# Kernel tuning notes

Hardware: AMD Instinct MI355X
Metric: run time of the kernel (lower is better)

The kernel has to match this reference:

```python
import jax, jax.numpy as jnp
import numpy as np

B, T, TS, J, D, H = 4, 512, 512, 17, 256, 8
CD = D // H
SCALE = CD ** -0.5


def setup_inputs() -> dict:
    key = jax.random.key(0)
    ks = jax.random.split(key, 7)
    return {
        "q": jax.random.normal(ks[0], (B, T, J, D), dtype=jnp.float32),
        "kv": jax.random.normal(ks[1], (B, TS, J, D), dtype=jnp.float32),
        "Wq": jax.random.normal(ks[2], (D, D), dtype=jnp.float32) * (D ** -0.5),
        "Wk": jax.random.normal(ks[3], (D, D), dtype=jnp.float32) * (D ** -0.5),
        "Wv": jax.random.normal(ks[4], (D, D), dtype=jnp.float32) * (D ** -0.5),
        "Wp": jax.random.normal(ks[5], (D, D), dtype=jnp.float32) * (D ** -0.5),
        "bp": jnp.zeros((D,), dtype=jnp.float32),
    }


def reference(q, kv, Wq, Wk, Wv, Wp, bp):
    b, t, j, d = q.shape
    t_sup = kv.shape[1]
    h, cd = H, CD
    # linear projections (torch Linear: x @ W^T), split heads -> [b,h,j,t,cd]
    qh = (q @ Wq.T).reshape(b, t, j, h, cd).transpose(0, 3, 2, 1, 4)
    kh = (kv @ Wk.T).reshape(b, t_sup, j, h, cd).transpose(0, 3, 2, 1, 4)
    vh = (kv @ Wv.T).reshape(b, t_sup, j, h, cd).transpose(0, 3, 2, 1, 4)
    # full attention matrix over temporal axes: [b,h,j,t,t_sup]
    scores = jnp.einsum("bhjtc,bhjsc->bhjts", qh, kh) * SCALE
    attn = jax.nn.softmax(scores, axis=-1)
    out = jnp.einsum("bhjts,bhjsc->bhjtc", attn, vh)
    out = out.transpose(0, 3, 2, 1, 4).reshape(b, t, j, d)  # [b,t,j,d]
    return out @ Wp.T + bp
```

## Files before the change

kernel.cpp:

```cpp
#include <hip/hip_runtime.h>
#include <hip/hip_bf16.h>

#define BB 4
#define TT 512
#define JJ 17
#define DD 256
#define HH 8
#define MROWS (BB*TT*JJ)
#define SZE ((size_t)MROWS * DD)
#define WSZ (DD*DD)
#define QSCALE 0.2550265247510319f
#define RST (17*256)

typedef short v8s __attribute__((ext_vector_type(8)));
typedef float v4f __attribute__((ext_vector_type(4)));

__device__ __forceinline__ unsigned short f2bf(float f) {
    union { float f; unsigned int u; } c; c.f = f;
    unsigned int u = c.u;
    return (unsigned short)((u + 0x7FFF + ((u >> 16) & 1)) >> 16);
}
__device__ __forceinline__ unsigned int pkbf(float lo, float hi) {
    union { float f; unsigned int u; } a, b; a.f = lo; b.f = hi;
    return __builtin_amdgcn_perm(b.u + 0x8000u, a.u + 0x8000u, 0x07060302u);
}
__device__ __forceinline__ float fexp2(float x) {
    return __builtin_amdgcn_exp2f(x);
}

__device__ __forceinline__ void gld16(const unsigned short* g, unsigned short* l) {
    __builtin_amdgcn_global_load_lds(
        (const __attribute__((address_space(1))) void*)g,
        (__attribute__((address_space(3))) void*)l,
        16, 0, 0);
}

__global__ __launch_bounds__(256) void prep_kernel(
    const float* __restrict__ q, const float* __restrict__ kv,
    const float* __restrict__ Wq, const float* __restrict__ Wk,
    const float* __restrict__ Wv, const float* __restrict__ Wp,
    unsigned short* __restrict__ qb, unsigned short* __restrict__ kvb,
    unsigned short* __restrict__ Wqb, unsigned short* __restrict__ Wkb,
    unsigned short* __restrict__ Wvb, unsigned short* __restrict__ Wpb)
{
    size_t i = ((size_t)blockIdx.x * 256 + threadIdx.x) * 8;
    const float* src; unsigned short* dst; size_t off; float scale = 1.f;
    if (i < SZE)            { src = q;  dst = qb;  off = i;        scale = QSCALE; }
    else if (i < 2 * SZE)   { src = kv; dst = kvb; off = i - SZE; }
    else {
        size_t k = i - 2 * SZE;
        int w = (int)(k >> 16);
        off = k & (WSZ - 1);
        src = (w == 0) ? Wq : (w == 1) ? Wk : (w == 2) ? Wv : Wp;
        dst = (w == 0) ? Wqb : (w == 1) ? Wkb : (w == 2) ? Wvb : Wpb;
    }
    float4 x0 = *(const float4*)(src + off);
    float4 x1 = *(const float4*)(src + off + 4);
    union { unsigned short s[8]; int4 v; } u;
    u.s[0] = f2bf(x0.x * scale); u.s[1] = f2bf(x0.y * scale);
    u.s[2] = f2bf(x0.z * scale); u.s[3] = f2bf(x0.w * scale);
    u.s[4] = f2bf(x1.x * scale); u.s[5] = f2bf(x1.y * scale);
    u.s[6] = f2bf(x1.z * scale); u.s[7] = f2bf(x1.w * scale);
    *(int4*)(dst + off) = u.v;
}

__global__ __launch_bounds__(512) void gemm_kernel(
    const unsigned short* __restrict__ A0,
    const unsigned short* __restrict__ A1,
    const unsigned short* __restrict__ A2,
    const unsigned short* __restrict__ W0,
    const unsigned short* __restrict__ W1,
    const unsigned short* __restrict__ W2,
    unsigned short* __restrict__ Y0,
    unsigned short* __restrict__ Y1,
    unsigned short* __restrict__ Y2)
{
    const int z = blockIdx.y;
    const unsigned short* A = (z == 0) ? A0 : (z == 1) ? A1 : A2;
    const unsigned short* W = (z == 0) ? W0 : (z == 1) ? W1 : W2;
    unsigned short* Y       = (z == 0) ? Y0 : (z == 1) ? Y1 : Y2;

    const int bm = blockIdx.x;

    __shared__ unsigned short As[2][128 * 32];
    __shared__ unsigned short Bs[2][256 * 32];

    const int tid  = threadIdx.x;
    const int wv   = tid >> 6;
    const int lane = tid & 63;
    const int wm   = wv & 1;
    const int wn   = wv >> 1;
    const int quad = lane >> 4;
    const int l16  = lane & 15;

    const int s     = lane >> 2;
    const int chunk = lane & 3;
    const int fsw   = (s ^ (s >> 2)) & 3;
    const int cg    = chunk ^ fsw;
    const int srow  = wv * 16 + s;
    const unsigned short* gA  = A + (size_t)(bm * 128 + srow) * 256 + cg * 8;
    const unsigned short* gB0 = W + (size_t)srow * 256 + cg * 8;
    const unsigned short* gB1 = W + (size_t)(128 + srow) * 256 + cg * 8;
    unsigned short* lA  = &As[0][wv * 512 + lane * 8];
    unsigned short* lB0 = &Bs[0][wv * 512 + lane * 8];
    unsigned short* lB1 = &Bs[0][4096 + wv * 512 + lane * 8];

    const int rch8 = (quad ^ ((l16 ^ (l16 >> 2)) & 3)) * 8;

    v4f acc[4][4] = {};

    gld16(gA,  lA);
    gld16(gB0, lB0);
    gld16(gB1, lB1);
    __syncthreads();

    for (int kt = 0; kt < 8; ++kt) {
        const int cur = kt & 1;
        if (kt < 7) {
            const int nk = (kt + 1) * 32;
            const int nb = cur ^ 1;
            gld16(gA  + nk, lA  + nb * 4096);
            gld16(gB0 + nk, lB0 + nb * 8192);
            gld16(gB1 + nk, lB1 + nb * 8192);
        }
        v8s a[4], b[4];
        #pragma unroll
        for (int i = 0; i < 4; ++i)
            a[i] = *(const v8s*)(&As[cur][(wm * 64 + i * 16 + l16) * 32 + rch8]);
        #pragma unroll
        for (int j = 0; j < 4; ++j)
            b[j] = *(const v8s*)(&Bs[cur][(wn * 64 + j * 16 + l16) * 32 + rch8]);
        #pragma unroll
        for (int i = 0; i < 4; ++i)
            #pragma unroll
            for (int j = 0; j < 4; ++j)
                acc[i][j] = __builtin_amdgcn_mfma_f32_16x16x32_bf16(
                    a[i], b[j], acc[i][j], 0, 0, 0);
        __syncthreads();
    }

    #pragma unroll
    for (int i = 0; i < 4; ++i)
        #pragma unroll
        for (int j = 0; j < 4; ++j)
            #pragma unroll
            for (int r = 0; r < 4; ++r) {
                int gm = bm * 128 + wm * 64 + i * 16 + quad * 4 + r;
                int gn = wn * 64 + j * 16 + l16;
                Y[(size_t)gm * 256 + gn] = f2bf(acc[i][j][r]);
            }
}

__global__ __launch_bounds__(256) void gemmo_kernel(
    const unsigned short* __restrict__ A,
    const unsigned short* __restrict__ W,
    const float* __restrict__ bias,
    float* __restrict__ out)
{
    const int bm = blockIdx.x;

    __shared__ unsigned short As[2][64 * 32];
    __shared__ unsigned short Bs[2][256 * 32];

    const int tid  = threadIdx.x;
    const int lane = tid & 63;
    const int wn   = tid >> 6;
    const int quad = lane >> 4;
    const int l16  = lane & 15;

    const int arow  = tid >> 2;
    const int chunk = tid & 3;
    const int cgA   = (chunk ^ ((arow ^ (arow >> 2)) & 3)) * 8;
    const unsigned short* gA = A + (size_t)(bm * 64 + arow) * 256 + cgA;
    const unsigned short* gB = W + (size_t)arow * 256 + cgA;
    unsigned short* lA = &As[0][tid * 8];
    unsigned short* lB = &Bs[0][tid * 8];

    const int rch8 = (quad ^ ((l16 ^ (l16 >> 2)) & 3)) * 8;

    v4f acc[4][4] = {};

    gld16(gA, lA);
    #pragma unroll
    for (int p = 0; p < 4; ++p)
        gld16(gB + (size_t)p * 64 * 256, lB + p * 2048);
    __syncthreads();

    for (int kt = 0; kt < 8; ++kt) {
        const int cur = kt & 1;
        if (kt < 7) {
            const int nk = (kt + 1) * 32;
            const int nb = cur ^ 1;
            gld16(gA + nk, lA + nb * 2048);
            #pragma unroll
            for (int p = 0; p < 4; ++p)
                gld16(gB + (size_t)p * 64 * 256 + nk, lB + nb * 8192 + p * 2048);
        }
        v8s a[4], b[4];
        #pragma unroll
        for (int i = 0; i < 4; ++i)
            a[i] = *(const v8s*)(&As[cur][(i * 16 + l16) * 32 + rch8]);
        #pragma unroll
        for (int j = 0; j < 4; ++j)
            b[j] = *(const v8s*)(&Bs[cur][(wn * 64 + j * 16 + l16) * 32 + rch8]);
        #pragma unroll
        for (int i = 0; i < 4; ++i)
            #pragma unroll
            for (int j = 0; j < 4; ++j)
                acc[i][j] = __builtin_amdgcn_mfma_f32_16x16x32_bf16(
                    a[i], b[j], acc[i][j], 0, 0, 0);
        __syncthreads();
    }

    #pragma unroll
    for (int i = 0; i < 4; ++i)
        #pragma unroll
        for (int j = 0; j < 4; ++j)
            #pragma unroll
            for (int r = 0; r < 4; ++r) {
                int gm = bm * 64 + i * 16 + quad * 4 + r;
                int gn = wn * 64 + j * 16 + l16;
                out[(size_t)gm * 256 + gn] = acc[i][j][r] + bias[gn];
            }
}

#define VST 136
#define PST 72

__global__ __launch_bounds__(256) void attn_kernel(
    const unsigned short* __restrict__ Qp,
    const unsigned short* __restrict__ Kp,
    const unsigned short* __restrict__ Vp,
    unsigned short* __restrict__ Att)
{
    const int id  = blockIdx.x;
    const int bjh = (id & 7) | ((id >> 5) << 3);
    const int qt  = (id >> 3) & 3;
    const int h   = bjh & 7;
    const int bj  = bjh >> 3;
    const int j   = bj % 17;
    const int b_  = bj / 17;

    __shared__ unsigned short Ks[128 * 40];
    __shared__ unsigned short Vs[32 * VST];
    __shared__ unsigned short Ps[128 * PST];
    __shared__ float Ls[128];

    const int tid  = threadIdx.x;
    const int wave = tid >> 6;
    const int lane = tid & 63;
    const int quad = lane >> 4;
    const int l16  = lane & 15;

    const int base0 = b_ * 512 * RST + j * 256 + h * 32;

    v8s qa[2];
    #pragma unroll
    for (int fi = 0; fi < 2; ++fi)
        qa[fi] = *(const v8s*)(
            Qp + base0 + (qt * 128 + wave * 32 + fi * 16 + l16) * RST + quad * 8);

    float lacc[2] = {0.f, 0.f};
    v4f accO[2][2] = {};

    for (int kc = 0; kc < 4; ++kc) {
        __syncthreads();
        #pragma unroll
        for (int c = 0; c < 2; ++c) {
            int krow = wave * 16 + l16 + c * 64;
            *(int4*)(&Ks[krow * 40 + quad * 8]) = *(const int4*)(
                Kp + base0 + (kc * 128 + krow) * RST + quad * 8);
        }
        #pragma unroll
        for (int c = 0; c < 2; ++c) {
            int idx  = c * 256 + tid;
            int srow = idx >> 2;
            int cd0  = (idx & 3) << 3;
            int xof  = (((srow >> 3) ^ (cd0 >> 3)) << 3) + (srow & 7);
            union { int4 v; unsigned short s[8]; } u;
            u.v = *(const int4*)(
                Vp + base0 + (kc * 128 + srow) * RST + cd0);
            #pragma unroll
            for (int i = 0; i < 8; ++i)
                Vs[(cd0 + i) * VST + xof] = u.s[i];
        }
        __syncthreads();

        #pragma unroll
        for (int half = 0; half < 2; ++half) {
            v4f accST[4][2] = {};
            __builtin_amdgcn_s_setprio(1);
            #pragma unroll
            for (int si = 0; si < 4; ++si) {
                v8s kb = *(const v8s*)(&Ks[((half * 4 + si) * 16 + l16) * 40 + quad * 8]);
                #pragma unroll
                for (int fi = 0; fi < 2; ++fi)
                    accST[si][fi] = __builtin_amdgcn_mfma_f32_16x16x32_bf16(
                        kb, qa[fi], accST[si][fi], 0, 0, 0);
            }
            __builtin_amdgcn_s_setprio(0);
            #pragma unroll
            for (int fi = 0; fi < 2; ++fi) {
                int prow = (wave * 32 + fi * 16 + l16) * PST;
                #pragma unroll
                for (int si = 0; si < 4; ++si) {
                    float p0 = fexp2(accST[si][fi][0]);
                    float p1 = fexp2(accST[si][fi][1]);
                    float p2 = fexp2(accST[si][fi][2]);
                    float p3 = fexp2(accST[si][fi][3]);
                    lacc[fi] += (p0 + p1) + (p2 + p3);
                    uint2 pk;
                    pk.x = pkbf(p0, p1);
                    pk.y = pkbf(p2, p3);
                    *(uint2*)(&Ps[prow + si * 16 + quad * 4]) = pk;
                }
            }
            asm volatile("s_waitcnt lgkmcnt(0)" ::: "memory");

            __builtin_amdgcn_s_setprio(1);
            #pragma unroll
            for (int ks = 0; ks < 2; ++ks) {
                v8s pa[2];
                #pragma unroll
                for (int fi = 0; fi < 2; ++fi)
                    pa[fi] = *(const v8s*)(&Ps[(wave * 32 + fi * 16 + l16) * PST +
                                               ks * 32 + quad * 8]);
                #pragma unroll
                for (int nj = 0; nj < 2; ++nj) {
                    int cd  = nj * 16 + l16;
                    int blk = (half * 8 + ks * 4 + quad) ^ (cd >> 3);
                    v8s vb = *(const v8s*)(&Vs[cd * VST + (blk << 3)]);
                    #pragma unroll
                    for (int fi = 0; fi < 2; ++fi)
                        accO[fi][nj] = __builtin_amdgcn_mfma_f32_16x16x32_bf16(
                            pa[fi], vb, accO[fi][nj], 0, 0, 0);
                }
            }
            __builtin_amdgcn_s_setprio(0);
        }
    }

    #pragma unroll
    for (int fi = 0; fi < 2; ++fi) {
        float lv = lacc[fi];
        lv += __shfl_xor(lv, 16);
        lv += __shfl_xor(lv, 32);
        if (quad == 0) Ls[wave * 32 + fi * 16 + l16] = lv;
    }
    asm volatile("s_waitcnt lgkmcnt(0)" ::: "memory");

    #pragma unroll
    for (int fi = 0; fi < 2; ++fi) {
        float4 lv = *(float4*)(&Ls[wave * 32 + fi * 16 + quad * 4]);
        float rl[4] = {1.f / lv.x, 1.f / lv.y, 1.f / lv.z, 1.f / lv.w};
        #pragma unroll
        for (int nj = 0; nj < 2; ++nj) {
            #pragma unroll
            for (int r = 0; r < 4; ++r) {
                int trow = qt * 128 + wave * 32 + fi * 16 + quad * 4 + r;
                int cd   = nj * 16 + l16;
                float v  = accO[fi][nj][r] * rl[r];
                Att[(size_t)(base0 + trow * RST + cd)] = f2bf(v);
            }
        }
    }
}

extern "C" void kernel_launch(void* const* d_in, const int* in_sizes, int n_in,
                              void* d_out, int out_size, void* d_ws, size_t ws_size,
                              hipStream_t stream) {
    const float* q  = (const float*)d_in[0];
    const float* kv = (const float*)d_in[1];
    const float* Wq = (const float*)d_in[2];
    const float* Wk = (const float*)d_in[3];
    const float* Wv = (const float*)d_in[4];
    const float* Wp = (const float*)d_in[5];
    const float* bp = (const float*)d_in[6];

    unsigned short* ws  = (unsigned short*)d_ws;
    unsigned short* Qp  = ws;
    unsigned short* Kp  = ws + SZE;
    unsigned short* Vp  = ws + 2 * SZE;
    unsigned short* qb  = ws + 3 * SZE;
    unsigned short* kvb = ws + 4 * SZE;
    unsigned short* Wqb = ws + 5 * SZE;
    unsigned short* Wkb = Wqb + WSZ;
    unsigned short* Wvb = Wkb + WSZ;
    unsigned short* Wpb = Wvb + WSZ;
    unsigned short* Att = qb;
    float* out = (float*)d_out;

    prep_kernel<<<8832, 256, 0, stream>>>(q, kv, Wq, Wk, Wv, Wp,
                                          qb, kvb, Wqb, Wkb, Wvb, Wpb);
    gemm_kernel<<<dim3(272, 3), 512, 0, stream>>>(
        qb, kvb, kvb, Wqb, Wkb, Wvb, Qp, Kp, Vp);
    attn_kernel<<<dim3(2176), 256, 0, stream>>>(Qp, Kp, Vp, Att);
    gemmo_kernel<<<dim3(544), 256, 0, stream>>>(Att, Wpb, bp, out);
}
```

Baseline: 210.1 us.

## Fuse fp32-to-bf16 activation conversion into QKV projection GEMM loads

The separate prep pass that converted q and kv to bf16 (and applied the Q scale) is removed. The QKV GEMM now reads fp32 activations directly, converts and scales them in registers, and writes them into the swizzled LDS buffer after the MFMA step so the conversion overlaps compute. Only the weight conversion stays as a small kernel. This saves a full read and write of two large activation tensors, but the A-tile loads become synchronous register loads instead of async global-to-LDS copies, and kv is read and converted twice, once for the K and once for the V projection.

```diff
diff --git a/kernel.cpp b/kernel.cpp
--- a/kernel.cpp
+++ b/kernel.cpp
@@ -35,39 +35,30 @@
         16, 0, 0);
 }
 
-__global__ __launch_bounds__(256) void prep_kernel(
-    const float* __restrict__ q, const float* __restrict__ kv,
+__global__ __launch_bounds__(256) void prepw_kernel(
     const float* __restrict__ Wq, const float* __restrict__ Wk,
     const float* __restrict__ Wv, const float* __restrict__ Wp,
-    unsigned short* __restrict__ qb, unsigned short* __restrict__ kvb,
     unsigned short* __restrict__ Wqb, unsigned short* __restrict__ Wkb,
     unsigned short* __restrict__ Wvb, unsigned short* __restrict__ Wpb)
 {
-    size_t i = ((size_t)blockIdx.x * 256 + threadIdx.x) * 8;
-    const float* src; unsigned short* dst; size_t off; float scale = 1.f;
-    if (i < SZE)            { src = q;  dst = qb;  off = i;        scale = QSCALE; }
-    else if (i < 2 * SZE)   { src = kv; dst = kvb; off = i - SZE; }
-    else {
-        size_t k = i - 2 * SZE;
-        int w = (int)(k >> 16);
-        off = k & (WSZ - 1);
-        src = (w == 0) ? Wq : (w == 1) ? Wk : (w == 2) ? Wv : Wp;
-        dst = (w == 0) ? Wqb : (w == 1) ? Wkb : (w == 2) ? Wvb : Wpb;
-    }
+    size_t k = ((size_t)blockIdx.x * 256 + threadIdx.x) * 8;
+    int w = (int)(k >> 16);
+    size_t off = k & (WSZ - 1);
+    const float* src = (w == 0) ? Wq : (w == 1) ? Wk : (w == 2) ? Wv : Wp;
+    unsigned short* dst = (w == 0) ? Wqb : (w == 1) ? Wkb : (w == 2) ? Wvb : Wpb;
     float4 x0 = *(const float4*)(src + off);
     float4 x1 = *(const float4*)(src + off + 4);
     union { unsigned short s[8]; int4 v; } u;
-    u.s[0] = f2bf(x0.x * scale); u.s[1] = f2bf(x0.y * scale);
-    u.s[2] = f2bf(x0.z * scale); u.s[3] = f2bf(x0.w * scale);
-    u.s[4] = f2bf(x1.x * scale); u.s[5] = f2bf(x1.y * scale);
-    u.s[6] = f2bf(x1.z * scale); u.s[7] = f2bf(x1.w * scale);
+    u.s[0] = f2bf(x0.x); u.s[1] = f2bf(x0.y);
+    u.s[2] = f2bf(x0.z); u.s[3] = f2bf(x0.w);
+    u.s[4] = f2bf(x1.x); u.s[5] = f2bf(x1.y);
+    u.s[6] = f2bf(x1.z); u.s[7] = f2bf(x1.w);
     *(int4*)(dst + off) = u.v;
 }
 
 __global__ __launch_bounds__(512) void gemm_kernel(
-    const unsigned short* __restrict__ A0,
-    const unsigned short* __restrict__ A1,
-    const unsigned short* __restrict__ A2,
+    const float* __restrict__ Aq,
+    const float* __restrict__ Akv,
     const unsigned short* __restrict__ W0,
     const unsigned short* __restrict__ W1,
     const unsigned short* __restrict__ W2,
@@ -76,7 +67,8 @@
     unsigned short* __restrict__ Y2)
 {
     const int z = blockIdx.y;
-    const unsigned short* A = (z == 0) ? A0 : (z == 1) ? A1 : A2;
+    const float* A          = (z == 0) ? Aq : Akv;
+    const float ascale      = (z == 0) ? QSCALE : 1.f;
     const unsigned short* W = (z == 0) ? W0 : (z == 1) ? W1 : W2;
     unsigned short* Y       = (z == 0) ? Y0 : (z == 1) ? Y1 : Y2;
 
@@ -93,33 +85,43 @@
     const int quad = lane >> 4;
     const int l16  = lane & 15;
 
-    const int s     = lane >> 2;
-    const int chunk = lane & 3;
-    const int fsw   = (s ^ (s >> 2)) & 3;
-    const int cg    = chunk ^ fsw;
-    const int srow  = wv * 16 + s;
-    const unsigned short* gA  = A + (size_t)(bm * 128 + srow) * 256 + cg * 8;
+    const int srow  = tid >> 2;
+    const int chunk = tid & 3;
+    const int s4    = srow & 15;
+    const int cg    = chunk ^ ((s4 ^ (s4 >> 2)) & 3);
+    const float* gA = A + (size_t)(bm * 128 + srow) * 256 + cg * 8;
     const unsigned short* gB0 = W + (size_t)srow * 256 + cg * 8;
     const unsigned short* gB1 = W + (size_t)(128 + srow) * 256 + cg * 8;
-    unsigned short* lA  = &As[0][wv * 512 + lane * 8];
-    unsigned short* lB0 = &Bs[0][wv * 512 + lane * 8];
-    unsigned short* lB1 = &Bs[0][4096 + wv * 512 + lane * 8];
+    unsigned short* lA  = &As[0][tid * 8];
+    unsigned short* lB0 = &Bs[0][tid * 8];
+    unsigned short* lB1 = &Bs[0][4096 + tid * 8];
 
     const int rch8 = (quad ^ ((l16 ^ (l16 >> 2)) & 3)) * 8;
 
     v4f acc[4][4] = {};
 
-    gld16(gA,  lA);
+    {
+        float4 a0 = *(const float4*)(gA);
+        float4 a1 = *(const float4*)(gA + 4);
+        union { unsigned short s[8]; int4 v; } ua;
+        ua.s[0] = f2bf(a0.x * ascale); ua.s[1] = f2bf(a0.y * ascale);
+        ua.s[2] = f2bf(a0.z * ascale); ua.s[3] = f2bf(a0.w * ascale);
+        ua.s[4] = f2bf(a1.x * ascale); ua.s[5] = f2bf(a1.y * ascale);
+        ua.s[6] = f2bf(a1.z * ascale); ua.s[7] = f2bf(a1.w * ascale);
+        *(int4*)(lA) = ua.v;
+    }
     gld16(gB0, lB0);
     gld16(gB1, lB1);
     __syncthreads();
 
     for (int kt = 0; kt < 8; ++kt) {
         const int cur = kt & 1;
+        const int nb  = cur ^ 1;
+        float4 a0, a1;
         if (kt < 7) {
             const int nk = (kt + 1) * 32;
-            const int nb = cur ^ 1;
-            gld16(gA  + nk, lA  + nb * 4096);
+            a0 = *(const float4*)(gA + nk);
+            a1 = *(const float4*)(gA + nk + 4);
             gld16(gB0 + nk, lB0 + nb * 8192);
             gld16(gB1 + nk, lB1 + nb * 8192);
         }
@@ -136,6 +138,14 @@
             for (int j = 0; j < 4; ++j)
                 acc[i][j] = __builtin_amdgcn_mfma_f32_16x16x32_bf16(
                     a[i], b[j], acc[i][j], 0, 0, 0);
+        if (kt < 7) {
+            union { unsigned short s[8]; int4 v; } ua;
+            ua.s[0] = f2bf(a0.x * ascale); ua.s[1] = f2bf(a0.y * ascale);
+            ua.s[2] = f2bf(a0.z * ascale); ua.s[3] = f2bf(a0.w * ascale);
+            ua.s[4] = f2bf(a1.x * ascale); ua.s[5] = f2bf(a1.y * ascale);
+            ua.s[6] = f2bf(a1.z * ascale); ua.s[7] = f2bf(a1.w * ascale);
+            *(int4*)(lA + nb * 4096) = ua.v;
+        }
         __syncthreads();
     }
 
@@ -381,19 +391,17 @@
     unsigned short* Qp  = ws;
     unsigned short* Kp  = ws + SZE;
     unsigned short* Vp  = ws + 2 * SZE;
-    unsigned short* qb  = ws + 3 * SZE;
-    unsigned short* kvb = ws + 4 * SZE;
-    unsigned short* Wqb = ws + 5 * SZE;
+    unsigned short* Att = ws + 3 * SZE;
+    unsigned short* Wqb = ws + 4 * SZE;
     unsigned short* Wkb = Wqb + WSZ;
     unsigned short* Wvb = Wkb + WSZ;
     unsigned short* Wpb = Wvb + WSZ;
-    unsigned short* Att = qb;
     float* out = (float*)d_out;
 
-    prep_kernel<<<8832, 256, 0, stream>>>(q, kv, Wq, Wk, Wv, Wp,
-                                          qb, kvb, Wqb, Wkb, Wvb, Wpb);
+    prepw_kernel<<<128, 256, 0, stream>>>(Wq, Wk, Wv, Wp,
+                                          Wqb, Wkb, Wvb, Wpb);
     gemm_kernel<<<dim3(272, 3), 512, 0, stream>>>(
-        qb, kvb, kvb, Wqb, Wkb, Wvb, Qp, Kp, Vp);
+        q, kv, Wqb, Wkb, Wvb, Qp, Kp, Vp);
     attn_kernel<<<dim3(2176), 256, 0, stream>>>(Qp, Kp, Vp, Att);
     gemmo_kernel<<<dim3(544), 256, 0, stream>>>(Att, Wpb, bp, out);
 }
```

Result: faster. 202.0 us (-3.9%).
